# Kernel tuning notes

Hardware: AMD Instinct MI355X
Metric: run time of the kernel (lower is better)

Reference implementation:

```python
import jax, jax.numpy as jnp
import numpy as np

LEFT, RIGHT = 64, 64  # left_size, right_size; hidden = LEFT*RIGHT = 4096


def _cayley(raw):
    """torch nn.utils.parametrizations.orthogonal(..., orthogonal_map='cayley',
    use_trivialization=False): A = triu(raw, 1); X = A - A^T (skew-symmetric);
    Q = (I - X/2)^{-1} (I + X/2)."""
    n = raw.shape[0]
    A = jnp.triu(raw, 1)
    X = A - A.T
    Id = jnp.eye(n, dtype=raw.dtype)
    return jnp.linalg.solve(Id - 0.5 * X, Id + 0.5 * X)


def setup_inputs() -> dict:
    key = jax.random.key(0)
    ks = jax.random.split(key, 8)
    B, S = 4, 2048
    H = LEFT * RIGHT
    inp = jax.random.normal(ks[0], (B, S, H), dtype=jnp.float32)
    raw_u_left = jax.random.normal(ks[1], (LEFT, LEFT), dtype=jnp.float32) * 0.02
    raw_v_left = jax.random.normal(ks[2], (LEFT, LEFT), dtype=jnp.float32) * 0.02
    raw_u_right = jax.random.normal(ks[3], (RIGHT, RIGHT), dtype=jnp.float32) * 0.02
    raw_v_right = jax.random.normal(ks[4], (RIGHT, RIGHT), dtype=jnp.float32) * 0.02
    diag_left = jnp.ones((LEFT,), dtype=jnp.float32)
    diag_right = jnp.ones((RIGHT,), dtype=jnp.float32)
    diag_scale = jnp.ones((H,), dtype=jnp.float32) + 0.01 * jax.random.normal(ks[5], (H,), dtype=jnp.float32)
    return {
        "inp": inp,
        "raw_u_left": raw_u_left,
        "raw_v_left": raw_v_left,
        "diag_left": diag_left,
        "raw_u_right": raw_u_right,
        "raw_v_right": raw_v_right,
        "diag_right": diag_right,
        "diag_scale": diag_scale,
        "inv_t": 0,
    }


def reference(inp, raw_u_left, raw_v_left, diag_left, raw_u_right, raw_v_right,
              diag_right, diag_scale, inv_t):
    # add_diag=True, use_diag=True path
    if inv_t:
        x = inp / diag_scale
        dl = 1.0 / diag_left
        dr = 1.0 / diag_right
    else:
        x = inp * diag_scale
        dl = diag_left
        dr = diag_right
    # Cayley-parametrized orthogonal factors
    Ul = _cayley(raw_u_left)
    Vl = _cayley(raw_v_left)
    Ur = _cayley(raw_u_right)
    Vr = _cayley(raw_v_right)
    # SVD-style reconstruction: M = U @ diag(d) @ V^T
    ML = (Ul * dl[None, :]) @ Vl.T  # [LEFT, LEFT]
    MR = (Ur * dr[None, :]) @ Vr.T  # [RIGHT, RIGHT]
    # Kronecker matmul: view last dim as [LEFT, RIGHT], out = ML^T @ X @ MR
    orig_shape = x.shape
    xb = x.reshape(-1, LEFT, RIGHT)  # [B*S, LEFT, RIGHT]
    out = jnp.einsum('bij,ik,jl->bkl', xb, ML, MR)
    return out.reshape(orig_shape)
```

## Files before the change

### kernel.cpp

```cpp
#include <hip/hip_runtime.h>
#include <hip/hip_bf16.h>

typedef short short8 __attribute__((ext_vector_type(8)));
typedef float f32x4 __attribute__((ext_vector_type(4)));
typedef float f32x16 __attribute__((ext_vector_type(16)));
typedef unsigned int u32x4 __attribute__((ext_vector_type(4)));

#define HID 4096
#define CST 68

#define LGKM0 do { asm volatile("s_waitcnt lgkmcnt(0)" ::: "memory"); \
                   __builtin_amdgcn_sched_barrier(0); } while (0)

__device__ __forceinline__ unsigned short f2bf(float f) {
    unsigned int u = __float_as_uint(f);
    u = (u + 0x7FFFu + ((u >> 16) & 1u)) >> 16;
    return (unsigned short)u;
}

__device__ __forceinline__ f32x4 mm4(const float* SA, const float* SB, int i, int j0) {
    f32x4 acc = {0.f, 0.f, 0.f, 0.f};
#pragma unroll 8
    for (int k = 0; k < 64; ++k) {
        float a = SA[i * CST + k];
        acc += a * *reinterpret_cast<const f32x4*>(SB + k * CST + j0);
    }
    return acc;
}

__global__ __launch_bounds__(1024) void cayley_build_kernel(
    const float* __restrict__ rul, const float* __restrict__ rvl, const float* __restrict__ dl,
    const float* __restrict__ rur, const float* __restrict__ rvr, const float* __restrict__ dr,
    const int* __restrict__ invt,
    unsigned short* __restrict__ plp, unsigned short* __restrict__ mrp)
{
    __shared__ __align__(16) float Yw[64 * CST], Aw[64 * CST], Pw[64 * CST];
    __shared__ __align__(16) float Qw[64 * CST], QTw[64 * CST];
    __shared__ float dd[64];

    const float* ru; const float* rv; const float* dv; unsigned short* ob;
    if (blockIdx.x == 0) { ru = rul; rv = rvl; dv = dl; ob = plp; }
    else                 { ru = rur; rv = rvr; dv = dr; ob = mrp; }

    const int tid = threadIdx.x;
    const int i = tid >> 4;
    const int j0 = (tid & 15) << 2;

    for (int pass = 0; pass < 2; ++pass) {
        const float* raw = (pass == 0) ? ru : rv;
#pragma unroll
        for (int q = 0; q < 4; ++q) {
            int j = j0 + q;
            float v = 0.f;
            if (j > i)      v =  raw[i * 64 + j];
            else if (j < i) v = -raw[j * 64 + i];
            Yw[i * CST + j] = 0.5f * v;
        }
        __syncthreads();
        f32x4 a = mm4(Yw, Yw, i, j0);
        __syncthreads();
        *reinterpret_cast<f32x4*>(Aw + i * CST + j0) = a;
        *reinterpret_cast<f32x4*>(Pw + i * CST + j0) =
            a + *reinterpret_cast<const f32x4*>(Yw + i * CST + j0);
        __syncthreads();
        a = mm4(Pw, Aw, i, j0);
        __syncthreads();
        *reinterpret_cast<f32x4*>(Pw + i * CST + j0) += a;
        __syncthreads();
        a = mm4(Aw, Aw, i, j0);
        __syncthreads();
        *reinterpret_cast<f32x4*>(Aw + i * CST + j0) = a;
        __syncthreads();
        a = mm4(Pw, Aw, i, j0);
        __syncthreads();
        f32x4 p = *reinterpret_cast<const f32x4*>(Pw + i * CST + j0) + a;
#pragma unroll
        for (int q = 0; q < 4; ++q) {
            int j = j0 + q;
            float qv = ((i == j) ? 1.f : 0.f) + 2.f * p[q];
            if (pass == 0) Qw[i * CST + j]  = qv;
            else           QTw[j * CST + i] = qv;
        }
        __syncthreads();
    }
    if (tid < 64) { float d = dv[tid]; dd[tid] = (invt[0] != 0) ? (1.0f / d) : d; }
    __syncthreads();

    f32x4 m = {0.f, 0.f, 0.f, 0.f};
#pragma unroll 8
    for (int j = 0; j < 64; ++j) {
        float aa = Qw[i * CST + j] * dd[j];
        m += aa * *reinterpret_cast<const f32x4*>(QTw + j * CST + j0);
    }
    const int kt = i >> 4, hh = (i >> 3) & 1, e = i & 7;
#pragma unroll
    for (int q = 0; q < 4; ++q) {
        int j = j0 + q;
        unsigned short v = f2bf(m[q]);
        int dst;
        if (blockIdx.x == 0)
            dst = (((j >> 5) * 4 + kt) * 64 + (j & 31) + 32 * hh) * 8 + e;
        else
            dst = ((kt * 2 + (j >> 5)) * 64 + (j & 31) + 32 * hh) * 8 + e;
        ob[dst] = v;
    }
}

__global__ __launch_bounds__(256, 4) void kron_kernel(
    const float* __restrict__ inp, const float* __restrict__ ds,
    const unsigned short* __restrict__ plp, const unsigned short* __restrict__ mrp,
    const int* __restrict__ invt, float* __restrict__ out, int ntok)
{
    __shared__ __align__(16) unsigned char sbuf[4][8192];
    const int w = threadIdx.x >> 6;
    const int lane = threadIdx.x & 63;
    const int r = lane & 31;
    const int h = lane >> 5;
    unsigned char* S = sbuf[w];

    const int t = blockIdx.x * 4 + w;
    if (t >= ntok) return;
    const bool inv = (invt[0] != 0);
    const float* xt = inp + (size_t)t * HID;

#pragma unroll
    for (int s = 0; s < 8; ++s) {
        const int fi = s * 512 + lane * 8;
        f32x4 x0 = *reinterpret_cast<const f32x4*>(xt + fi);
        f32x4 x1 = *reinterpret_cast<const f32x4*>(xt + fi + 4);
        f32x4 d0 = *reinterpret_cast<const f32x4*>(ds + fi);
        f32x4 d1 = *reinterpret_cast<const f32x4*>(ds + fi + 4);
        if (inv) {
#pragma unroll
            for (int e = 0; e < 4; ++e) { x0[e] /= d0[e]; x1[e] /= d1[e]; }
        } else {
            x0 *= d0; x1 *= d1;
        }
        short8 f;
#pragma unroll
        for (int e = 0; e < 4; ++e) {
            f[e]     = (short)f2bf(x0[e]);
            f[e + 4] = (short)f2bf(x1[e]);
        }
        const int m = s * 8 + (lane >> 3);
        const int c = lane & 7;
        *reinterpret_cast<short8*>(S + ((m * 8 + (c ^ (m & 7))) << 4)) = f;
    }
    LGKM0;

    unsigned int zs[4][8];
#pragma unroll
    for (int nt = 0; nt < 2; ++nt) {
        short8 b1[4];
#pragma unroll
        for (int kt = 0; kt < 4; ++kt)
            b1[kt] = *reinterpret_cast<const short8*>(
                mrp + ((kt * 2 + nt) * 64 + lane) * 8);
#pragma unroll
        for (int mt = 0; mt < 2; ++mt) {
            short8 a1[4];
#pragma unroll
            for (int kt = 0; kt < 4; ++kt)
                a1[kt] = *reinterpret_cast<const short8*>(
                    S + (((32 * mt + r) * 8 + ((2 * kt + h) ^ (r & 7))) << 4));
            f32x16 acc = {0.f};
#pragma unroll
            for (int kt = 0; kt < 4; ++kt)
                acc = __builtin_amdgcn_mfma_f32_32x32x16_bf16(a1[kt], b1[kt], acc, 0, 0, 0);
            unsigned int q[8];
#pragma unroll
            for (int p = 0; p < 8; ++p)
                q[p] = (unsigned int)f2bf(acc[2 * p]) |
                       ((unsigned int)f2bf(acc[2 * p + 1]) << 16);
            auto s02 = __builtin_amdgcn_permlane32_swap(q[0], q[2], false, false);
            auto s13 = __builtin_amdgcn_permlane32_swap(q[1], q[3], false, false);
            auto s46 = __builtin_amdgcn_permlane32_swap(q[4], q[6], false, false);
            auto s57 = __builtin_amdgcn_permlane32_swap(q[5], q[7], false, false);
            unsigned int* z = zs[mt * 2 + nt];
            z[0] = s02[0]; z[1] = s13[0]; z[2] = s02[1]; z[3] = s13[1];
            z[4] = s46[0]; z[5] = s57[0]; z[6] = s46[1]; z[7] = s57[1];
        }
    }

    float* op = out + (size_t)t * HID;
#pragma unroll
    for (int mt2 = 0; mt2 < 2; ++mt2) {
        short8 a2[4];
#pragma unroll
        for (int kt = 0; kt < 4; ++kt)
            a2[kt] = *reinterpret_cast<const short8*>(
                plp + ((mt2 * 4 + kt) * 64 + lane) * 8);
#pragma unroll
        for (int nt2 = 0; nt2 < 2; ++nt2) {
            f32x16 y = {0.f};
#pragma unroll
            for (int kt2 = 0; kt2 < 4; ++kt2) {
                const unsigned int* z = zs[(kt2 >> 1) * 2 + nt2];
                const int kb = (kt2 & 1) * 4;
                union { u32x4 u; short8 s; } cv;
                cv.u[0] = z[kb + 0]; cv.u[1] = z[kb + 1];
                cv.u[2] = z[kb + 2]; cv.u[3] = z[kb + 3];
                y = __builtin_amdgcn_mfma_f32_32x32x16_bf16(a2[kt2], cv.s, y, 0, 0, 0);
            }
#pragma unroll
            for (int g = 0; g < 16; ++g) {
                const int k = 32 * mt2 + (g & 3) + 8 * (g >> 2) + 4 * h;
                op[k * 64 + 32 * nt2 + r] = y[g];
            }
        }
    }
}

extern "C" void kernel_launch(void* const* d_in, const int* in_sizes, int n_in,
                              void* d_out, int out_size, void* d_ws, size_t ws_size,
                              hipStream_t stream) {
    const float* inp = (const float*)d_in[0];
    const float* rul = (const float*)d_in[1];
    const float* rvl = (const float*)d_in[2];
    const float* dl  = (const float*)d_in[3];
    const float* rur = (const float*)d_in[4];
    const float* rvr = (const float*)d_in[5];
    const float* dr  = (const float*)d_in[6];
    const float* ds  = (const float*)d_in[7];
    const int*   invt = (const int*)d_in[8];
    float* out = (float*)d_out;

    unsigned short* plp = (unsigned short*)d_ws;
    unsigned short* mrp = plp + 4096;

    const int ntok = in_sizes[0] / HID;

    hipLaunchKernelGGL(cayley_build_kernel, dim3(2), dim3(1024), 0, stream,
                       rul, rvl, dl, rur, rvr, dr, invt, plp, mrp);
    const int nblk = (ntok + 3) / 4;
    hipLaunchKernelGGL(kron_kernel, dim3(nblk), dim3(256), 0, stream,
                       inp, ds, plp, mrp, invt, out, ntok);
}
```

Before: 83.43 us.

## Split input scaling and bf16 conversion into a separate pre-pass kernel

Adds a grid-stride kernel that scales the input by diag_scale and writes a packed bf16 copy to workspace. A new kron kernel then reads its MFMA A operands straight from that bf16 buffer, with no LDS staging or swizzle. The aim is to decouple the memory-bound conversion from the MFMA kernel and raise its occupancy. The cost is an extra full write and read of a half-size intermediate plus one more launch, which adds HBM traffic. It falls back to the old kernel when the workspace is too small.

After: 109.8 us. +31.6%, slower.

```diff
diff --git a/kernel.cpp b/kernel.cpp
--- a/kernel.cpp
+++ b/kernel.cpp
@@ -26,6 +26,33 @@
         acc += a * *reinterpret_cast<const f32x4*>(SB + k * CST + j0);
     }
     return acc;
+}
+
+__global__ __launch_bounds__(256) void cvt_kernel(
+    const f32x4* __restrict__ x, const f32x4* __restrict__ dsq,
+    u32x4* __restrict__ wq, const int* __restrict__ invt, size_t npair)
+{
+    const bool inv = (invt[0] != 0);
+    size_t i = (size_t)blockIdx.x * 256 + threadIdx.x;
+    const size_t st = (size_t)gridDim.x * 256;
+    for (size_t p = i; p < npair; p += st) {
+        f32x4 x0 = x[2 * p];
+        f32x4 x1 = x[2 * p + 1];
+        f32x4 d0 = dsq[(2 * p) & 1023];
+        f32x4 d1 = dsq[(2 * p + 1) & 1023];
+        if (inv) {
+#pragma unroll
+            for (int e = 0; e < 4; ++e) { x0[e] /= d0[e]; x1[e] /= d1[e]; }
+        } else {
+            x0 *= d0; x1 *= d1;
+        }
+        u32x4 pk;
+        pk[0] = (unsigned int)f2bf(x0[0]) | ((unsigned int)f2bf(x0[1]) << 16);
+        pk[1] = (unsigned int)f2bf(x0[2]) | ((unsigned int)f2bf(x0[3]) << 16);
+        pk[2] = (unsigned int)f2bf(x1[0]) | ((unsigned int)f2bf(x1[1]) << 16);
+        pk[3] = (unsigned int)f2bf(x1[2]) | ((unsigned int)f2bf(x1[3]) << 16);
+        wq[p] = pk;
+    }
 }
 
 __global__ __launch_bounds__(1024) void cayley_build_kernel(
@@ -103,6 +130,82 @@
         else
             dst = ((kt * 2 + (j >> 5)) * 64 + (j & 31) + 32 * hh) * 8 + e;
         ob[dst] = v;
+    }
+}
+
+__global__ __launch_bounds__(256, 4) void kron2_kernel(
+    const unsigned short* __restrict__ Wb,
+    const unsigned short* __restrict__ plp, const unsigned short* __restrict__ mrp,
+    float* __restrict__ out, int ntok)
+{
+    const int lane = threadIdx.x & 63;
+    const int r = lane & 31;
+    const int h = lane >> 5;
+
+    const int t = blockIdx.x * 4 + (threadIdx.x >> 6);
+    if (t >= ntok) return;
+    const unsigned short* wt = Wb + (size_t)t * HID;
+
+    unsigned int zs[4][8];
+#pragma unroll
+    for (int nt = 0; nt < 2; ++nt) {
+        short8 b1[4];
+#pragma unroll
+        for (int kt = 0; kt < 4; ++kt)
+            b1[kt] = *reinterpret_cast<const short8*>(
+                mrp + ((kt * 2 + nt) * 64 + lane) * 8);
+#pragma unroll
+        for (int mt = 0; mt < 2; ++mt) {
+            short8 a1[4];
+#pragma unroll
+            for (int kt = 0; kt < 4; ++kt)
+                a1[kt] = *reinterpret_cast<const short8*>(
+                    wt + (32 * mt + r) * 64 + 16 * kt + 8 * h);
+            f32x16 acc = {0.f};
+#pragma unroll
+            for (int kt = 0; kt < 4; ++kt)
+                acc = __builtin_amdgcn_mfma_f32_32x32x16_bf16(a1[kt], b1[kt], acc, 0, 0, 0);
+            unsigned int q[8];
+#pragma unroll
+            for (int p = 0; p < 8; ++p)
+                q[p] = (unsigned int)f2bf(acc[2 * p]) |
+                       ((unsigned int)f2bf(acc[2 * p + 1]) << 16);
+            auto s02 = __builtin_amdgcn_permlane32_swap(q[0], q[2], false, false);
+            auto s13 = __builtin_amdgcn_permlane32_swap(q[1], q[3], false, false);
+            auto s46 = __builtin_amdgcn_permlane32_swap(q[4], q[6], false, false);
+            auto s57 = __builtin_amdgcn_permlane32_swap(q[5], q[7], false, false);
+            unsigned int* z = zs[mt * 2 + nt];
+            z[0] = s02[0]; z[1] = s13[0]; z[2] = s02[1]; z[3] = s13[1];
+            z[4] = s46[0]; z[5] = s57[0]; z[6] = s46[1]; z[7] = s57[1];
+        }
+    }
+
+    float* op = out + (size_t)t * HID;
+#pragma unroll
+    for (int mt2 = 0; mt2 < 2; ++mt2) {
+        short8 a2[4];
+#pragma unroll
+        for (int kt = 0; kt < 4; ++kt)
+            a2[kt] = *reinterpret_cast<const short8*>(
+                plp + ((mt2 * 4 + kt) * 64 + lane) * 8);
+#pragma unroll
+        for (int nt2 = 0; nt2 < 2; ++nt2) {
+            f32x16 y = {0.f};
+#pragma unroll
+            for (int kt2 = 0; kt2 < 4; ++kt2) {
+                const unsigned int* z = zs[(kt2 >> 1) * 2 + nt2];
+                const int kb = (kt2 & 1) * 4;
+                union { u32x4 u; short8 s; } cv;
+                cv.u[0] = z[kb + 0]; cv.u[1] = z[kb + 1];
+                cv.u[2] = z[kb + 2]; cv.u[3] = z[kb + 3];
+                y = __builtin_amdgcn_mfma_f32_32x32x16_bf16(a2[kt2], cv.s, y, 0, 0, 0);
+            }
+#pragma unroll
+            for (int g = 0; g < 16; ++g) {
+                const int k = 32 * mt2 + (g & 3) + 8 * (g >> 2) + 4 * h;
+                op[k * 64 + 32 * nt2 + r] = y[g];
+            }
+        }
     }
 }
 
@@ -229,10 +332,24 @@
     unsigned short* mrp = plp + 4096;
 
     const int ntok = in_sizes[0] / HID;
+    const size_t wbytes = (size_t)ntok * HID * 2;
+    const size_t woff = 1u << 20;
 
     hipLaunchKernelGGL(cayley_build_kernel, dim3(2), dim3(1024), 0, stream,
                        rul, rvl, dl, rur, rvr, dr, invt, plp, mrp);
-    const int nblk = (ntok + 3) / 4;
-    hipLaunchKernelGGL(kron_kernel, dim3(nblk), dim3(256), 0, stream,
-                       inp, ds, plp, mrp, invt, out, ntok);
-}
+
+    if (ws_size >= woff + wbytes) {
+        unsigned short* Wb = (unsigned short*)((char*)d_ws + woff);
+        const size_t npair = (size_t)ntok * 512;
+        hipLaunchKernelGGL(cvt_kernel, dim3(2048), dim3(256), 0, stream,
+                           (const f32x4*)inp, (const f32x4*)ds,
+                           (u32x4*)Wb, invt, npair);
+        const int nblk = (ntok + 3) / 4;
+        hipLaunchKernelGGL(kron2_kernel, dim3(nblk), dim3(256), 0, stream,
+                           Wb, plp, mrp, out, ntok);
+    } else {
+        const int nblk = (ntok + 3) / 4;
+        hipLaunchKernelGGL(kron_kernel, dim3(nblk), dim3(256), 0, stream,
+                           inp, ds, plp, mrp, invt, out, ntok);
+    }
+}
```

## Split input scaling/bf16 conversion into separate pass and pipeline multi-token MFMA kernel

Applied to the files above, without the earlier changes.

Adds a conversion kernel that applies diag_scale and writes a bf16 copy of the input to workspace. A new kron kernel keeps both factor matrices in registers and processes four tokens per wave, loading the A operands straight from the bf16 buffer with double-buffered register prefetch instead of staging through LDS. This adds an extra global round trip (write 2 bytes and read 2 bytes per element) and a kernel launch, in exchange for less LDS traffic and better overlap of loads with MFMA. The original kernel is kept as a fallback when the workspace is too small.

Measured after the change: 145.0 us. +73.8%, slower.

```diff
diff --git a/kernel.cpp b/kernel.cpp
--- a/kernel.cpp
+++ b/kernel.cpp
@@ -104,6 +104,138 @@
             dst = ((kt * 2 + (j >> 5)) * 64 + (j & 31) + 32 * hh) * 8 + e;
         ob[dst] = v;
     }
+}
+
+__global__ __launch_bounds__(1024) void cvt_kernel(
+    const float* __restrict__ x, const float* __restrict__ dsv,
+    u32x4* __restrict__ wq, const int* __restrict__ invt, int ntok)
+{
+    const int gt = blockIdx.x * 1024 + threadIdx.x;
+    const int o  = (gt & 511) * 8;
+    const int g  = gt >> 9;
+    const int ng = (gridDim.x * 1024) >> 9;
+    const bool inv = (invt[0] != 0);
+
+    f32x4 d0 = *reinterpret_cast<const f32x4*>(dsv + o);
+    f32x4 d1 = *reinterpret_cast<const f32x4*>(dsv + o + 4);
+    if (inv) {
+#pragma unroll
+        for (int e = 0; e < 4; ++e) { d0[e] = 1.0f / d0[e]; d1[e] = 1.0f / d1[e]; }
+    }
+
+    for (int t = g; t < ntok; t += ng) {
+        const float* xt = x + (size_t)t * HID + o;
+        f32x4 x0 = *reinterpret_cast<const f32x4*>(xt);
+        f32x4 x1 = *reinterpret_cast<const f32x4*>(xt + 4);
+        x0 *= d0; x1 *= d1;
+        u32x4 pk;
+        pk[0] = (unsigned int)f2bf(x0[0]) | ((unsigned int)f2bf(x0[1]) << 16);
+        pk[1] = (unsigned int)f2bf(x0[2]) | ((unsigned int)f2bf(x0[3]) << 16);
+        pk[2] = (unsigned int)f2bf(x1[0]) | ((unsigned int)f2bf(x1[1]) << 16);
+        pk[3] = (unsigned int)f2bf(x1[2]) | ((unsigned int)f2bf(x1[3]) << 16);
+        wq[((size_t)t * HID + o) >> 3] = pk;
+    }
+}
+
+#define LOADA(A, T) do { \
+    const unsigned short* _wt = Wb + (size_t)(T) * HID; \
+    _Pragma("unroll") \
+    for (int mt = 0; mt < 2; ++mt) \
+    _Pragma("unroll") \
+    for (int kt = 0; kt < 4; ++kt) \
+        A[mt * 4 + kt] = *reinterpret_cast<const short8*>( \
+            _wt + (32 * mt + r) * 64 + 16 * kt + 8 * h); \
+} while (0)
+
+#define BODY(A, T) do { \
+    unsigned int zs[4][8]; \
+    _Pragma("unroll") \
+    for (int nt = 0; nt < 2; ++nt) { \
+        _Pragma("unroll") \
+        for (int mt = 0; mt < 2; ++mt) { \
+            f32x16 acc = {0.f}; \
+            _Pragma("unroll") \
+            for (int kt = 0; kt < 4; ++kt) \
+                acc = __builtin_amdgcn_mfma_f32_32x32x16_bf16( \
+                    A[mt * 4 + kt], b1[kt * 2 + nt], acc, 0, 0, 0); \
+            unsigned int q[8]; \
+            _Pragma("unroll") \
+            for (int p = 0; p < 8; ++p) \
+                q[p] = (unsigned int)f2bf(acc[2 * p]) | \
+                       ((unsigned int)f2bf(acc[2 * p + 1]) << 16); \
+            auto s02 = __builtin_amdgcn_permlane32_swap(q[0], q[2], false, false); \
+            auto s13 = __builtin_amdgcn_permlane32_swap(q[1], q[3], false, false); \
+            auto s46 = __builtin_amdgcn_permlane32_swap(q[4], q[6], false, false); \
+            auto s57 = __builtin_amdgcn_permlane32_swap(q[5], q[7], false, false); \
+            unsigned int* z = zs[mt * 2 + nt]; \
+            z[0] = s02[0]; z[1] = s13[0]; z[2] = s02[1]; z[3] = s13[1]; \
+            z[4] = s46[0]; z[5] = s57[0]; z[6] = s46[1]; z[7] = s57[1]; \
+        } \
+    } \
+    float* op = out + (size_t)(T) * HID; \
+    _Pragma("unroll") \
+    for (int mt2 = 0; mt2 < 2; ++mt2) { \
+        _Pragma("unroll") \
+        for (int nt2 = 0; nt2 < 2; ++nt2) { \
+            f32x16 y = {0.f}; \
+            _Pragma("unroll") \
+            for (int kt2 = 0; kt2 < 4; ++kt2) { \
+                const unsigned int* z = zs[(kt2 >> 1) * 2 + nt2]; \
+                const int kb = (kt2 & 1) * 4; \
+                union { u32x4 u; short8 s; } cv; \
+                cv.u[0] = z[kb + 0]; cv.u[1] = z[kb + 1]; \
+                cv.u[2] = z[kb + 2]; cv.u[3] = z[kb + 3]; \
+                y = __builtin_amdgcn_mfma_f32_32x32x16_bf16( \
+                    a2[mt2 * 4 + kt2], cv.s, y, 0, 0, 0); \
+            } \
+            _Pragma("unroll") \
+            for (int g = 0; g < 16; ++g) { \
+                const int k = 32 * mt2 + (g & 3) + 8 * (g >> 2) + 4 * h; \
+                op[k * 64 + 32 * nt2 + r] = y[g]; \
+            } \
+        } \
+    } \
+} while (0)
+
+__global__ __launch_bounds__(256, 2) void kron2_kernel(
+    const unsigned short* __restrict__ Wb,
+    const unsigned short* __restrict__ plp, const unsigned short* __restrict__ mrp,
+    float* __restrict__ out, int ntok)
+{
+    const int lane = threadIdx.x & 63;
+    const int r = lane & 31;
+    const int h = lane >> 5;
+
+    short8 b1[8], a2[8];
+#pragma unroll
+    for (int kt = 0; kt < 4; ++kt)
+#pragma unroll
+        for (int nt = 0; nt < 2; ++nt)
+            b1[kt * 2 + nt] = *reinterpret_cast<const short8*>(
+                mrp + ((kt * 2 + nt) * 64 + lane) * 8);
+#pragma unroll
+    for (int mt = 0; mt < 2; ++mt)
+#pragma unroll
+        for (int kt = 0; kt < 4; ++kt)
+            a2[mt * 4 + kt] = *reinterpret_cast<const short8*>(
+                plp + ((mt * 4 + kt) * 64 + lane) * 8);
+
+    const int wv = blockIdx.x * 4 + (threadIdx.x >> 6);
+    const int t0 = wv * 4;
+    if (t0 >= ntok) return;
+    const bool h1 = (t0 + 1) < ntok;
+    const bool h2 = (t0 + 2) < ntok;
+    const bool h3 = (t0 + 3) < ntok;
+
+    short8 aA[8], aB[8];
+    LOADA(aA, t0);
+    if (h1) LOADA(aB, t0 + 1);
+    BODY(aA, t0);
+    if (h2) LOADA(aA, t0 + 2);
+    if (h1) BODY(aB, t0 + 1);
+    if (h3) LOADA(aB, t0 + 3);
+    if (h2) BODY(aA, t0 + 2);
+    if (h3) BODY(aB, t0 + 3);
 }
 
 __global__ __launch_bounds__(256, 4) void kron_kernel(
@@ -229,10 +361,22 @@
     unsigned short* mrp = plp + 4096;
 
     const int ntok = in_sizes[0] / HID;
+    const size_t wbytes = (size_t)ntok * HID * 2;
+    const size_t woff = 1u << 20;
 
     hipLaunchKernelGGL(cayley_build_kernel, dim3(2), dim3(1024), 0, stream,
                        rul, rvl, dl, rur, rvr, dr, invt, plp, mrp);
-    const int nblk = (ntok + 3) / 4;
-    hipLaunchKernelGGL(kron_kernel, dim3(nblk), dim3(256), 0, stream,
-                       inp, ds, plp, mrp, invt, out, ntok);
-}
+
+    if (ws_size >= woff + wbytes) {
+        unsigned short* Wb = (unsigned short*)((char*)d_ws + woff);
+        hipLaunchKernelGGL(cvt_kernel, dim3(512), dim3(1024), 0, stream,
+                           inp, ds, (u32x4*)Wb, invt, ntok);
+        const int nblk2 = (ntok + 15) / 16;
+        hipLaunchKernelGGL(kron2_kernel, dim3(nblk2), dim3(256), 0, stream,
+                           Wb, plp, mrp, out, ntok);
+    } else {
+        const int nblk = (ntok + 3) / 4;
+        hipLaunchKernelGGL(kron_kernel, dim3(nblk), dim3(256), 0, stream,
+                           inp, ds, plp, mrp, invt, out, ntok);
+    }
+}
```

## Warp-specialize kron kernel into producer loaders and consumer MFMA warps

Applied to the files above, without the earlier changes.

Rewrites the kron kernel as a persistent-per-block pipeline. Two producer waves double-buffer fp32 token rows and the diag scale into swizzled LDS, while two consumer waves keep the Kronecker factors in registers and run both MFMA stages. Each block handles 16 tokens in 8 groups, so loads overlap with compute and the per-token factor reloads go away. In exchange, 80KB of LDS per block sharply limits occupancy, half the waves do no math, and a block barrier separates every group.

After: 82.74 us. No clear change (-0.8%).

```diff
diff --git a/kernel.cpp b/kernel.cpp
--- a/kernel.cpp
+++ b/kernel.cpp
@@ -8,9 +8,8 @@
 
 #define HID 4096
 #define CST 68
-
-#define LGKM0 do { asm volatile("s_waitcnt lgkmcnt(0)" ::: "memory"); \
-                   __builtin_amdgcn_sched_barrier(0); } while (0)
+#define NG  8
+#define TB  16
 
 __device__ __forceinline__ unsigned short f2bf(float f) {
     unsigned int u = __float_as_uint(f);
@@ -106,108 +105,168 @@
     }
 }
 
-__global__ __launch_bounds__(256, 4) void kron_kernel(
-    const float* __restrict__ inp, const float* __restrict__ ds,
+__global__ __launch_bounds__(256) void kron_pc_kernel(
+    const float* __restrict__ inp, const float* __restrict__ dsg,
     const unsigned short* __restrict__ plp, const unsigned short* __restrict__ mrp,
     const int* __restrict__ invt, float* __restrict__ out, int ntok)
 {
-    __shared__ __align__(16) unsigned char sbuf[4][8192];
+    extern __shared__ __align__(16) unsigned char L[];
+    float* dsb = reinterpret_cast<float*>(L + 65536);
+
     const int w = threadIdx.x >> 6;
     const int lane = threadIdx.x & 63;
     const int r = lane & 31;
     const int h = lane >> 5;
-    unsigned char* S = sbuf[w];
-
-    const int t = blockIdx.x * 4 + w;
-    if (t >= ntok) return;
+
+    const int base = blockIdx.x * TB;
+    if (base >= ntok) return;
     const bool inv = (invt[0] != 0);
-    const float* xt = inp + (size_t)t * HID;
-
-#pragma unroll
-    for (int s = 0; s < 8; ++s) {
-        const int fi = s * 512 + lane * 8;
-        f32x4 x0 = *reinterpret_cast<const f32x4*>(xt + fi);
-        f32x4 x1 = *reinterpret_cast<const f32x4*>(xt + fi + 4);
-        f32x4 d0 = *reinterpret_cast<const f32x4*>(ds + fi);
-        f32x4 d1 = *reinterpret_cast<const f32x4*>(ds + fi + 4);
-        if (inv) {
-#pragma unroll
-            for (int e = 0; e < 4; ++e) { x0[e] /= d0[e]; x1[e] /= d1[e]; }
+
+    short8 b1[8], a2[8];
+
+    if (w >= 2) {
+        const int p = w - 2;
+#pragma unroll
+        for (int it = 0; it < 8; ++it) {
+            const int s = (p * 8 + it) * 64 + lane;
+            const int sg = s ^ ((s >> 4) & 15);
+            *reinterpret_cast<f32x4*>(dsb + sg * 4) =
+                *reinterpret_cast<const f32x4*>(dsg + s * 4);
+        }
+        const int t0 = base + p;
+        if (t0 < ntok) {
+            float* dst = reinterpret_cast<float*>(L + (0 * 2 + p) * 16384);
+            const float* src = inp + (size_t)t0 * HID;
+#pragma unroll
+            for (int it = 0; it < 16; ++it) {
+                const int s = it * 64 + lane;
+                const int sg = s ^ ((s >> 4) & 15);
+                *reinterpret_cast<f32x4*>(dst + sg * 4) =
+                    *reinterpret_cast<const f32x4*>(src + s * 4);
+            }
+        }
+        asm volatile("s_waitcnt vmcnt(0) lgkmcnt(0)" ::: "memory");
+    } else {
+#pragma unroll
+        for (int kt = 0; kt < 4; ++kt)
+#pragma unroll
+            for (int nt = 0; nt < 2; ++nt)
+                b1[kt * 2 + nt] = *reinterpret_cast<const short8*>(
+                    mrp + ((kt * 2 + nt) * 64 + lane) * 8);
+#pragma unroll
+        for (int mt = 0; mt < 2; ++mt)
+#pragma unroll
+            for (int kt = 0; kt < 4; ++kt)
+                a2[mt * 4 + kt] = *reinterpret_cast<const short8*>(
+                    plp + ((mt * 4 + kt) * 64 + lane) * 8);
+    }
+    __builtin_amdgcn_sched_barrier(0);
+    __builtin_amdgcn_s_barrier();
+
+    for (int g = 0; g < NG; ++g) {
+        if (w < 2) {
+            const int t = base + g * 2 + w;
+            if (t < ntok) {
+                const float* xf = reinterpret_cast<const float*>(
+                    L + ((g & 1) * 2 + w) * 16384);
+
+                short8 a1f[8];
+#pragma unroll
+                for (int mt = 0; mt < 2; ++mt)
+#pragma unroll
+                    for (int kt = 0; kt < 4; ++kt) {
+                        const int R = 32 * mt + r;
+                        const int c0 = 4 * kt + 2 * h;
+                        const int u0 = 16 * R + (c0 ^ (R & 15));
+                        const int u1 = 16 * R + ((c0 + 1) ^ (R & 15));
+                        f32x4 x0 = *reinterpret_cast<const f32x4*>(xf + u0 * 4);
+                        f32x4 x1 = *reinterpret_cast<const f32x4*>(xf + u1 * 4);
+                        f32x4 d0 = *reinterpret_cast<const f32x4*>(dsb + u0 * 4);
+                        f32x4 d1 = *reinterpret_cast<const f32x4*>(dsb + u1 * 4);
+                        if (inv) {
+#pragma unroll
+                            for (int e = 0; e < 4; ++e) { x0[e] /= d0[e]; x1[e] /= d1[e]; }
+                        } else {
+                            x0 *= d0; x1 *= d1;
+                        }
+                        short8 f;
+#pragma unroll
+                        for (int e = 0; e < 4; ++e) {
+                            f[e]     = (short)f2bf(x0[e]);
+                            f[e + 4] = (short)f2bf(x1[e]);
+                        }
+                        a1f[mt * 4 + kt] = f;
+                    }
+
+                unsigned int zs[4][8];
+#pragma unroll
+                for (int nt = 0; nt < 2; ++nt)
+#pragma unroll
+                    for (int mt = 0; mt < 2; ++mt) {
+                        f32x16 acc = {0.f};
+#pragma unroll
+                        for (int kt = 0; kt < 4; ++kt)
+                            acc = __builtin_amdgcn_mfma_f32_32x32x16_bf16(
+                                a1f[mt * 4 + kt], b1[kt * 2 + nt], acc, 0, 0, 0);
+                        unsigned int q[8];
+#pragma unroll
+                        for (int p = 0; p < 8; ++p)
+                            q[p] = (unsigned int)f2bf(acc[2 * p]) |
+                                   ((unsigned int)f2bf(acc[2 * p + 1]) << 16);
+                        auto s02 = __builtin_amdgcn_permlane32_swap(q[0], q[2], false, false);
+                        auto s13 = __builtin_amdgcn_permlane32_swap(q[1], q[3], false, false);
+                        auto s46 = __builtin_amdgcn_permlane32_swap(q[4], q[6], false, false);
+                        auto s57 = __builtin_amdgcn_permlane32_swap(q[5], q[7], false, false);
+                        unsigned int* z = zs[mt * 2 + nt];
+                        z[0] = s02[0]; z[1] = s13[0]; z[2] = s02[1]; z[3] = s13[1];
+                        z[4] = s46[0]; z[5] = s57[0]; z[6] = s46[1]; z[7] = s57[1];
+                    }
+
+                float* op = out + (size_t)t * HID;
+#pragma unroll
+                for (int mt2 = 0; mt2 < 2; ++mt2)
+#pragma unroll
+                    for (int nt2 = 0; nt2 < 2; ++nt2) {
+                        f32x16 y = {0.f};
+#pragma unroll
+                        for (int kt2 = 0; kt2 < 4; ++kt2) {
+                            const unsigned int* z = zs[(kt2 >> 1) * 2 + nt2];
+                            const int kb = (kt2 & 1) * 4;
+                            union { u32x4 u; short8 s; } cv;
+                            cv.u[0] = z[kb + 0]; cv.u[1] = z[kb + 1];
+                            cv.u[2] = z[kb + 2]; cv.u[3] = z[kb + 3];
+                            y = __builtin_amdgcn_mfma_f32_32x32x16_bf16(
+                                a2[mt2 * 4 + kt2], cv.s, y, 0, 0, 0);
+                        }
+#pragma unroll
+                        for (int gg = 0; gg < 16; ++gg) {
+                            const int k = 32 * mt2 + (gg & 3) + 8 * (gg >> 2) + 4 * h;
+                            op[k * 64 + 32 * nt2 + r] = y[gg];
+                        }
+                    }
+            }
+            asm volatile("s_waitcnt lgkmcnt(0)" ::: "memory");
         } else {
-            x0 *= d0; x1 *= d1;
-        }
-        short8 f;
-#pragma unroll
-        for (int e = 0; e < 4; ++e) {
-            f[e]     = (short)f2bf(x0[e]);
-            f[e + 4] = (short)f2bf(x1[e]);
-        }
-        const int m = s * 8 + (lane >> 3);
-        const int c = lane & 7;
-        *reinterpret_cast<short8*>(S + ((m * 8 + (c ^ (m & 7))) << 4)) = f;
-    }
-    LGKM0;
-
-    unsigned int zs[4][8];
-#pragma unroll
-    for (int nt = 0; nt < 2; ++nt) {
-        short8 b1[4];
-#pragma unroll
-        for (int kt = 0; kt < 4; ++kt)
-            b1[kt] = *reinterpret_cast<const short8*>(
-                mrp + ((kt * 2 + nt) * 64 + lane) * 8);
-#pragma unroll
-        for (int mt = 0; mt < 2; ++mt) {
-            short8 a1[4];
-#pragma unroll
-            for (int kt = 0; kt < 4; ++kt)
-                a1[kt] = *reinterpret_cast<const short8*>(
-                    S + (((32 * mt + r) * 8 + ((2 * kt + h) ^ (r & 7))) << 4));
-            f32x16 acc = {0.f};
-#pragma unroll
-            for (int kt = 0; kt < 4; ++kt)
-                acc = __builtin_amdgcn_mfma_f32_32x32x16_bf16(a1[kt], b1[kt], acc, 0, 0, 0);
-            unsigned int q[8];
-#pragma unroll
-            for (int p = 0; p < 8; ++p)
-                q[p] = (unsigned int)f2bf(acc[2 * p]) |
-                       ((unsigned int)f2bf(acc[2 * p + 1]) << 16);
-            auto s02 = __builtin_amdgcn_permlane32_swap(q[0], q[2], false, false);
-            auto s13 = __builtin_amdgcn_permlane32_swap(q[1], q[3], false, false);
-            auto s46 = __builtin_amdgcn_permlane32_swap(q[4], q[6], false, false);
-            auto s57 = __builtin_amdgcn_permlane32_swap(q[5], q[7], false, false);
-            unsigned int* z = zs[mt * 2 + nt];
-            z[0] = s02[0]; z[1] = s13[0]; z[2] = s02[1]; z[3] = s13[1];
-            z[4] = s46[0]; z[5] = s57[0]; z[6] = s46[1]; z[7] = s57[1];
-        }
-    }
-
-    float* op = out + (size_t)t * HID;
-#pragma unroll
-    for (int mt2 = 0; mt2 < 2; ++mt2) {
-        short8 a2[4];
-#pragma unroll
-        for (int kt = 0; kt < 4; ++kt)
-            a2[kt] = *reinterpret_cast<const short8*>(
-                plp + ((mt2 * 4 + kt) * 64 + lane) * 8);
-#pragma unroll
-        for (int nt2 = 0; nt2 < 2; ++nt2) {
-            f32x16 y = {0.f};
-#pragma unroll
-            for (int kt2 = 0; kt2 < 4; ++kt2) {
-                const unsigned int* z = zs[(kt2 >> 1) * 2 + nt2];
-                const int kb = (kt2 & 1) * 4;
-                union { u32x4 u; short8 s; } cv;
-                cv.u[0] = z[kb + 0]; cv.u[1] = z[kb + 1];
-                cv.u[2] = z[kb + 2]; cv.u[3] = z[kb + 3];
-                y = __builtin_amdgcn_mfma_f32_32x32x16_bf16(a2[kt2], cv.s, y, 0, 0, 0);
+            if (g + 1 < NG) {
+                const int p = w - 2;
+                const int t2 = base + (g + 1) * 2 + p;
+                if (t2 < ntok) {
+                    float* dst = reinterpret_cast<float*>(
+                        L + (((g + 1) & 1) * 2 + p) * 16384);
+                    const float* src = inp + (size_t)t2 * HID;
+#pragma unroll
+                    for (int it = 0; it < 16; ++it) {
+                        const int s = it * 64 + lane;
+                        const int sg = s ^ ((s >> 4) & 15);
+                        *reinterpret_cast<f32x4*>(dst + sg * 4) =
+                            *reinterpret_cast<const f32x4*>(src + s * 4);
+                    }
+                }
             }
-#pragma unroll
-            for (int g = 0; g < 16; ++g) {
-                const int k = 32 * mt2 + (g & 3) + 8 * (g >> 2) + 4 * h;
-                op[k * 64 + 32 * nt2 + r] = y[g];
-            }
-        }
+            asm volatile("s_waitcnt vmcnt(0) lgkmcnt(0)" ::: "memory");
+        }
+        __builtin_amdgcn_sched_barrier(0);
+        __builtin_amdgcn_s_barrier();
     }
 }
 
@@ -232,7 +291,7 @@
 
     hipLaunchKernelGGL(cayley_build_kernel, dim3(2), dim3(1024), 0, stream,
                        rul, rvl, dl, rur, rvr, dr, invt, plp, mrp);
-    const int nblk = (ntok + 3) / 4;
-    hipLaunchKernelGGL(kron_kernel, dim3(nblk), dim3(256), 0, stream,
+    const int nblk = (ntok + TB - 1) / TB;
+    hipLaunchKernelGGL(kron_pc_kernel, dim3(nblk), dim3(256), 81920, stream,
                        inp, ds, plp, mrp, invt, out, ntok);
 }
```
